# Kernel optimization log

Hardware: AMD Instinct MI355X
Metric: run time of the kernel (lower is better)

Reference implementation:

```python
import jax, jax.numpy as jnp
import numpy as np

B, T, E, H = 64, 577, 768, 64
GRID_H, GRID_W = 24, 24
NUM_PREFIX = 1
N = GRID_H * GRID_W  # 576 patches
EPS = 1e-5


def setup_inputs() -> dict:
    key = jax.random.key(0)
    ks = jax.random.split(key, 12)
    s = lambda k, shape, fan: jax.random.normal(k, shape, jnp.float32) / np.sqrt(fan)
    return {
        "x": jax.random.normal(ks[0], (B, T, E), jnp.float32),
        "w_q": s(ks[1], (E, H), E),
        "w_k": s(ks[2], (E, H), E),
        "w_v": s(ks[3], (E, H), E),
        "q_gamma": jnp.ones((H,), jnp.float32),
        "q_beta": jnp.zeros((H,), jnp.float32),
        "k_gamma": jnp.ones((H,), jnp.float32),
        "k_beta": jnp.zeros((H,), jnp.float32),
        "w_sigma": s(ks[4], (H, 2), H),
        "b_sigma": jnp.zeros((2,), jnp.float32),
        "w_alpha": s(ks[5], (H, 1), H),
        "b_alpha": jnp.zeros((1,), jnp.float32),
    }


def _layernorm(x, gamma, beta):
    mu = jnp.mean(x, axis=-1, keepdims=True)
    var = jnp.mean(jnp.square(x - mu), axis=-1, keepdims=True)
    return (x - mu) * jax.lax.rsqrt(var + EPS) * gamma + beta


def _grid_sq_dists():
    # coords[i] = (row, col) of patch i; squared coordinate differences [N, N]
    coords = jnp.stack(
        jnp.meshgrid(jnp.arange(GRID_H), jnp.arange(GRID_W), indexing="ij"), axis=-1
    ).reshape(N, 2).astype(jnp.float32)
    diff = coords[:, None, :] - coords[None, :, :]  # [N, N, 2]
    dy2 = jnp.square(diff[..., 0])  # row diff squared
    dx2 = jnp.square(diff[..., 1])  # col diff squared
    return dx2, dy2


def reference(x, w_q, w_k, w_v, q_gamma, q_beta, k_gamma, k_beta,
              w_sigma, b_sigma, w_alpha, b_alpha):
    q = _layernorm(x @ w_q, q_gamma, q_beta)  # [B, T, H]
    k = _layernorm(x @ w_k, k_gamma, k_beta)  # [B, T, H]
    v = x @ w_v                               # [B, T, H]

    sim = jnp.einsum("bqh,bkh->bqk", q, k)    # [B, T, T]

    q_nc = q[:, NUM_PREFIX:, :]               # [B, N, H]
    alpha = jax.nn.softplus(q_nc @ w_alpha + b_alpha)[..., 0]  # [B, N]
    sigma = jax.nn.sigmoid(q_nc @ w_sigma + b_sigma)           # [B, N, 2]
    sx = sigma[..., 0]  # [B, N]
    sy = sigma[..., 1]

    dx2, dy2 = _grid_sq_dists()  # [N, N] each
    # Gaussian decay bias: query-patch p controls sigma; [B, N, N]
    G = jnp.exp(
        -dx2[None] / (2.0 * jnp.square(sx)[:, :, None])
        - dy2[None] / (2.0 * jnp.square(sy)[:, :, None])
    )
    S = alpha[:, :, None] * G

    sim = sim.at[:, NUM_PREFIX:, NUM_PREFIX:].add(S)

    scale = jnp.sqrt(jnp.float32(H))
    attn = jax.nn.softmax(sim / scale, axis=-1)
    return attn @ v  # [B, T, H]
```

## Files before the change

kernel.cpp:

```cpp
#include <hip/hip_runtime.h>
#include <math.h>

#define B_ 64
#define T_ 577
#define E_ 768
#define H_ 64
#define N_ 576
#define GW_ 24

typedef float f32x4 __attribute__((ext_vector_type(4)));
typedef __bf16 bf16x8 __attribute__((ext_vector_type(8)));
typedef __bf16 bf16x4 __attribute__((ext_vector_type(4)));

__device__ inline void split_bf16(float f, __bf16& h, __bf16& l) {
  h = (__bf16)f;
  l = (__bf16)(f - (float)h);
}

__device__ inline float bperm_f(int byte_addr, float x) {
  return __int_as_float(__builtin_amdgcn_ds_bpermute(byte_addr, __float_as_int(x)));
}

#define GLOAD_LDS16(G, L)                                                     \
  __builtin_amdgcn_global_load_lds(                                           \
      (const __attribute__((address_space(1))) void*)(G),                     \
      (__attribute__((address_space(3))) void*)(L), 16, 0, 0)

__global__ __launch_bounds__(256) void prep_w_kernel(
    const float* __restrict__ wq, const float* __restrict__ wk, const float* __restrict__ wv,
    __bf16* __restrict__ wsw2)
{
  int t = blockIdx.x * 256 + threadIdx.x;
  if (t >= 24*192) return;
  int kc = t / 192, n = t - kc*192;
  const float* src = (n < 64) ? wq : ((n < 128) ? wk : wv);
  int nn = n & 63;
  int xb = (n & 3) ^ ((n >> 2) & 3);
  size_t cbase = (size_t)kc * 12288;
  #pragma unroll
  for (int g = 0; g < 4; ++g) {
    __bf16 hb[8], lb[8];
    #pragma unroll
    for (int j = 0; j < 8; ++j) {
      float f = src[(size_t)(kc*32 + g*8 + j)*64 + nn];
      split_bf16(f, hb[j], lb[j]);
    }
    int slot = n*4 + (g ^ xb);
    *(bf16x8*)(wsw2 + cbase + slot*8)        = *(bf16x8*)hb;
    *(bf16x8*)(wsw2 + cbase + 6144 + slot*8) = *(bf16x8*)lb;
  }
}

__global__ __launch_bounds__(256) void qkv_ln_kernel(
    const float* __restrict__ x, const __bf16* __restrict__ wsw2,
    const float* __restrict__ qg, const float* __restrict__ qb,
    const float* __restrict__ kg, const float* __restrict__ kb,
    const float* __restrict__ wsig, const float* __restrict__ bsig,
    const float* __restrict__ walp, const float* __restrict__ balp,
    float* __restrict__ qo, float* __restrict__ ko, float* __restrict__ vo,
    float* __restrict__ alo, float* __restrict__ sxo, float* __restrict__ syo)
{
  __shared__ __align__(16) float smem[64*193 + 256];
  __bf16* A_hi0 = (__bf16*)smem;
  __bf16* A_lo0 = A_hi0 + 2560;
  __bf16* A_hi1 = A_lo0 + 2560;
  __bf16* A_lo1 = A_hi1 + 2560;
  __bf16* B0    = A_lo1 + 2560;
  float (*Cs)[193] = (float (*)[193])smem;
  float* mu_q = smem + 64*193;
  float* rs_q = mu_q + 64;
  float* mu_k = rs_q + 64;
  float* rs_k = mu_k + 64;

  const int tid  = threadIdx.x;
  const int lane = tid & 63;
  const int w    = tid >> 6;
  const int quad = lane >> 4;
  const int m    = lane & 15;
  const int rowbase = blockIdx.x << 6;

  f32x4 acc[4][3];
  #pragma unroll
  for (int mt = 0; mt < 4; ++mt)
    #pragma unroll
    for (int nt = 0; nt < 3; ++nt)
      acc[mt][nt] = (f32x4){0.f, 0.f, 0.f, 0.f};

  const int kfrag = quad * 8;
  const int xl    = quad ^ (m & 3) ^ (m >> 2);

  float4 xr0, xr1;
  const int arow0 = tid >> 3,         ak0 = (tid & 7) * 4;
  const int arow1 = (tid + 256) >> 3, ak1 = (tid & 7) * 4;

  auto load_A = [&](int kc) {
    xr0 = *(const float4*)(x + (size_t)(rowbase + arow0)*E_ + kc*32 + ak0);
    xr1 = *(const float4*)(x + (size_t)(rowbase + arow1)*E_ + kc*32 + ak1);
  };
  auto store_A_to = [&](__bf16* AH, __bf16* AL) {
    __bf16 h0,l0,h1,l1,h2,l2,h3,l3;
    split_bf16(xr0.x,h0,l0); split_bf16(xr0.y,h1,l1);
    split_bf16(xr0.z,h2,l2); split_bf16(xr0.w,h3,l3);
    *(bf16x4*)&AH[arow0*40 + ak0] = (bf16x4){h0,h1,h2,h3};
    *(bf16x4*)&AL[arow0*40 + ak0] = (bf16x4){l0,l1,l2,l3};
    split_bf16(xr1.x,h0,l0); split_bf16(xr1.y,h1,l1);
    split_bf16(xr1.z,h2,l2); split_bf16(xr1.w,h3,l3);
    *(bf16x4*)&AH[arow1*40 + ak1] = (bf16x4){h0,h1,h2,h3};
    *(bf16x4*)&AL[arow1*40 + ak1] = (bf16x4){l0,l1,l2,l3};
  };
  auto issue_B = [&](int kc) {
    const size_t roff = (size_t)w * 1536;
    const __bf16* s_hi = wsw2 + (size_t)kc*12288 + roff + lane*8;
    const __bf16* s_lo = s_hi + 6144;
    __bf16* d_hi = B0 + roff;
    __bf16* d_lo = d_hi + 6144;
    #pragma unroll
    for (int j = 0; j < 3; ++j) {
      GLOAD_LDS16(s_hi + j*512, d_hi + j*512);
      GLOAD_LDS16(s_lo + j*512, d_lo + j*512);
    }
  };

  issue_B(0);
  load_A(0);
  store_A_to(A_hi0, A_lo0);
  load_A(1);
  __syncthreads();

  __bf16 *cA_hi = A_hi0, *cA_lo = A_lo0, *nA_hi = A_hi1, *nA_lo = A_lo1;

  #pragma unroll 1
  for (int kc = 0; kc < 24; ++kc) {
    bf16x8 bh[3], bl[3];
    #pragma unroll
    for (int nt = 0; nt < 3; ++nt) {
      int slotb = (w*48 + nt*16 + m)*4 + xl;
      bh[nt] = *(const bf16x8*)&B0[slotb*8];
      bl[nt] = *(const bf16x8*)&B0[6144 + slotb*8];
    }
    if (kc < 23) store_A_to(nA_hi, nA_lo);
    asm volatile("s_waitcnt lgkmcnt(0)" ::: "memory");
    __builtin_amdgcn_sched_barrier(0);
    if (kc < 23) issue_B(kc + 1);
    if (kc < 22) load_A(kc + 2);

    #pragma unroll
    for (int mt = 0; mt < 4; ++mt) {
      bf16x8 ah = *(const bf16x8*)&cA_hi[(mt*16 + m)*40 + kfrag];
      bf16x8 al = *(const bf16x8*)&cA_lo[(mt*16 + m)*40 + kfrag];
      #pragma unroll
      for (int nt = 0; nt < 3; ++nt) {
        acc[mt][nt] = __builtin_amdgcn_mfma_f32_16x16x32_bf16(ah, bh[nt], acc[mt][nt], 0, 0, 0);
        acc[mt][nt] = __builtin_amdgcn_mfma_f32_16x16x32_bf16(al, bh[nt], acc[mt][nt], 0, 0, 0);
        acc[mt][nt] = __builtin_amdgcn_mfma_f32_16x16x32_bf16(ah, bl[nt], acc[mt][nt], 0, 0, 0);
      }
    }
    __syncthreads();
    __bf16* t;
    t = cA_hi; cA_hi = nA_hi; nA_hi = t;
    t = cA_lo; cA_lo = nA_lo; nA_lo = t;
  }

  #pragma unroll
  for (int mt = 0; mt < 4; ++mt)
    #pragma unroll
    for (int nt = 0; nt < 3; ++nt) {
      int row = mt*16 + quad*4;
      int col = w*48 + nt*16 + m;
      Cs[row + 0][col] = acc[mt][nt].x;
      Cs[row + 1][col] = acc[mt][nt].y;
      Cs[row + 2][col] = acc[mt][nt].z;
      Cs[row + 3][col] = acc[mt][nt].w;
    }
  __syncthreads();

  if (tid < 64) {
    float s = 0.f;
    for (int h = 0; h < 64; ++h) s += Cs[tid][h];
    float mu = s * (1.f/64.f);
    float vs = 0.f;
    for (int h = 0; h < 64; ++h) { float d = Cs[tid][h] - mu; vs += d*d; }
    mu_q[tid] = mu;
    rs_q[tid] = rsqrtf(vs*(1.f/64.f) + 1e-5f);
  } else if (tid < 128) {
    int r = tid - 64;
    float s = 0.f;
    for (int h = 0; h < 64; ++h) s += Cs[r][64+h];
    float mu = s * (1.f/64.f);
    float vs = 0.f;
    for (int h = 0; h < 64; ++h) { float d = Cs[r][64+h] - mu; vs += d*d; }
    mu_k[r] = mu;
    rs_k[r] = rsqrtf(vs*(1.f/64.f) + 1e-5f);
  }
  __syncthreads();

  if (tid >= 192) {
    int r = tid - 192;
    int mrow = rowbase + r;
    int tindex = mrow % T_;
    if (tindex >= 1) {
      int bb = mrow / T_;
      int g = tindex - 1;
      float mu = mu_q[r], rs = rs_q[r];
      float za = 0.f, z0 = 0.f, z1 = 0.f;
      for (int h = 0; h < 64; ++h) {
        float qv = (Cs[r][h] - mu) * rs * qg[h] + qb[h];
        za += qv * walp[h];
        z0 += qv * wsig[2*h];
        z1 += qv * wsig[2*h+1];
      }
      za += balp[0]; z0 += bsig[0]; z1 += bsig[1];
      float al = fmaxf(za, 0.f) + log1pf(__expf(-fabsf(za)));
      float sx = 1.f/(1.f + __expf(-z0));
      float sy = 1.f/(1.f + __expf(-z1));
      alo[bb*N_ + g] = al;
      sxo[bb*N_ + g] = 0.5f/(sx*sx);
      syo[bb*N_ + g] = 0.5f/(sy*sy);
    }
  }
  for (int idx = tid; idx < 64*48; idx += 256) {
    int r = idx / 48, c4 = (idx - (idx/48)*48) * 4;
    size_t row = (size_t)rowbase + r;
    float4 val = make_float4(Cs[r][c4], Cs[r][c4+1], Cs[r][c4+2], Cs[r][c4+3]);
    if (c4 < 64) {
      float mu = mu_q[r], rs = rs_q[r];
      float4 o;
      o.x = (val.x - mu)*rs*qg[c4+0] + qb[c4+0];
      o.y = (val.y - mu)*rs*qg[c4+1] + qb[c4+1];
      o.z = (val.z - mu)*rs*qg[c4+2] + qb[c4+2];
      o.w = (val.w - mu)*rs*qg[c4+3] + qb[c4+3];
      *(float4*)(qo + row*64 + c4) = o;
    } else if (c4 < 128) {
      int h = c4 - 64;
      float mu = mu_k[r], rs = rs_k[r];
      float4 o;
      o.x = (val.x - mu)*rs*kg[h+0] + kb[h+0];
      o.y = (val.y - mu)*rs*kg[h+1] + kb[h+1];
      o.z = (val.z - mu)*rs*kg[h+2] + kb[h+2];
      o.w = (val.w - mu)*rs*kg[h+3] + kb[h+3];
      *(float4*)(ko + row*64 + h) = o;
    } else {
      *(float4*)(vo + row*64 + (c4-128)) = val;
    }
  }
}

__global__ __launch_bounds__(256, 4) void attn_kernel(
    const float* __restrict__ q, const float* __restrict__ k, const float* __restrict__ v,
    const float* __restrict__ ala, const float* __restrict__ sxa, const float* __restrict__ sya,
    float* __restrict__ out)
{
  __shared__ __align__(16) __bf16 sm[4*4608];
  __bf16* KH = sm;            __bf16* KL = sm + 4608;
  __bf16* VH = sm + 2*4608;   __bf16* VL = sm + 3*4608;

  const int tid  = threadIdx.x;
  const int lane = tid & 63;
  const int w    = tid >> 6;
  const int quad = lane >> 4;
  const int m    = lane & 15;

  const int f       = blockIdx.y * 10 + blockIdx.x;
  const int logical = (f & 7) * 80 + (f >> 3);
  const int b       = logical / 10;
  const int qt      = logical - b * 10;

  const float* qbase = q + (size_t)b * T_ * H_;
  const float* kbase = k + (size_t)b * T_ * H_;
  const float* vbase = v + (size_t)b * T_ * H_;

  const int  row    = qt*64 + w*16 + m;
  const int  rowc   = row < T_ ? row : T_ - 1;
  const bool qvalid = row < T_;
  const bool qhas   = (row >= 1) && qvalid;
  float al = 0.f, isx = 0.f, isy = 0.f, qr = 0.f, qc = 0.f;
  {
    int g = qhas ? row - 1 : 0;
    if (qhas) {
      al  = ala[b*N_ + g] * 0.125f;
      isx = sxa[b*N_ + g];
      isy = sya[b*N_ + g];
      int gr = g / GW_;
      qr = (float)gr;
      qc = (float)(g - gr*GW_);
    }
  }

  bf16x8 qh[2], ql[2];
  #pragma unroll
  for (int ks = 0; ks < 2; ++ks) {
    float4 f0 = *(const float4*)(qbase + (size_t)rowc*H_ + ks*32 + quad*8);
    float4 f1 = *(const float4*)(qbase + (size_t)rowc*H_ + ks*32 + quad*8 + 4);
    float fv[8] = {f0.x, f0.y, f0.z, f0.w, f1.x, f1.y, f1.z, f1.w};
    #pragma unroll
    for (int j = 0; j < 8; ++j) {
      float s = fv[j] * 0.125f;
      __bf16 h, l;
      split_bf16(s, h, l);
      qh[ks][j] = h;
      ql[ks][j] = l;
    }
  }

  float mo = -INFINITY, lsum = 0.f;
  f32x4 acc[4];
  #pragma unroll
  for (int nt = 0; nt < 4; ++nt) acc[nt] = (f32x4){0.f, 0.f, 0.f, 0.f};

  const int  addrA = ((2*(quad & 1))*16 + m) * 4;
  const int  addrB = addrA + 64;
  const bool hiNT  = quad >= 2;

  float4 kreg[4];
  float  vreg[16];
  const int d0 = tid & 15, k0 = (tid >> 4) * 4;

  auto load_kv = [&](int kt) {
    #pragma unroll
    for (int i = 0; i < 4; ++i) {
      int s = tid + 256*i;
      int key = s >> 4, c4 = (s & 15)*4;
      int kgl = kt*64 + key;
      int kcl = kgl < T_ ? kgl : T_ - 1;
      kreg[i] = *(const float4*)(kbase + (size_t)kcl*H_ + c4);
    }
    #pragma unroll
    for (int di = 0; di < 4; ++di)
      #pragma unroll
      for (int ki = 0; ki < 4; ++ki) {
        int kgl = kt*64 + k0 + ki;
        int kcl = kgl < T_ ? kgl : T_ - 1;
        vreg[di*4+ki] = vbase[(size_t)kcl*H_ + d0 + 16*di];
      }
  };
  auto store_kv = [&]() {
    #pragma unroll
    for (int i = 0; i < 4; ++i) {
      int s = tid + 256*i;
      int key = s >> 4, c4 = (s & 15)*4;
      __bf16 h0,l0,h1,l1,h2,l2,h3,l3;
      split_bf16(kreg[i].x,h0,l0); split_bf16(kreg[i].y,h1,l1);
      split_bf16(kreg[i].z,h2,l2); split_bf16(kreg[i].w,h3,l3);
      *(bf16x4*)&KH[key*72 + c4] = (bf16x4){h0,h1,h2,h3};
      *(bf16x4*)&KL[key*72 + c4] = (bf16x4){l0,l1,l2,l3};
    }
    #pragma unroll
    for (int di = 0; di < 4; ++di) {
      int dim = d0 + 16*di;
      __bf16 h0,l0,h1,l1,h2,l2,h3,l3;
      split_bf16(vreg[di*4+0],h0,l0); split_bf16(vreg[di*4+1],h1,l1);
      split_bf16(vreg[di*4+2],h2,l2); split_bf16(vreg[di*4+3],h3,l3);
      *(bf16x4*)&VH[dim*72 + k0] = (bf16x4){h0,h1,h2,h3};
      *(bf16x4*)&VL[dim*72 + k0] = (bf16x4){l0,l1,l2,l3};
    }
  };

  load_kv(0);
  #pragma unroll 1
  for (int kt = 0; kt < 10; ++kt) {
    __syncthreads();
    store_kv();
    __syncthreads();
    if (kt < 9) load_kv(kt + 1);

    float s_[4][4];
    #pragma unroll
    for (int nt = 0; nt < 4; ++nt) {
      f32x4 sac = (f32x4){0.f, 0.f, 0.f, 0.f};
      #pragma unroll
      for (int ks = 0; ks < 2; ++ks) {
        const int ko_ = ks*32 + quad*8;
        bf16x8 kh = *(const bf16x8*)&KH[(nt*16 + m)*72 + ko_];
        bf16x8 kl = *(const bf16x8*)&KL[(nt*16 + m)*72 + ko_];
        sac = __builtin_amdgcn_mfma_f32_16x16x32_bf16(kh, qh[ks], sac, 0, 0, 0);
        sac = __builtin_amdgcn_mfma_f32_16x16x32_bf16(kl, qh[ks], sac, 0, 0, 0);
        sac = __builtin_amdgcn_mfma_f32_16x16x32_bf16(kh, ql[ks], sac, 0, 0, 0);
      }
      s_[nt][0] = sac.x; s_[nt][1] = sac.y; s_[nt][2] = sac.z; s_[nt][3] = sac.w;
    }

    #pragma unroll
    for (int nt = 0; nt < 4; ++nt) {
      #pragma unroll
      for (int reg = 0; reg < 4; ++reg) {
        int key = kt*64 + nt*16 + quad*4 + reg;
        float sval = s_[nt][reg];
        float kgf = (float)(key - 1);
        float krf = floorf(kgf * (1.0f/24.0f));
        float kcf = kgf - 24.f*krf;
        float dx = qc - kcf, dy = qr - krf;
        float bias = al * __expf(-(dx*dx*isx + dy*dy*isy));
        bool khas = (key >= 1) && (key < T_);
        sval += (khas && qhas) ? bias : 0.f;
        s_[nt][reg] = (key < T_) ? sval : -1e30f;
      }
    }

    float mx = s_[0][0];
    #pragma unroll
    for (int nt = 0; nt < 4; ++nt)
      #pragma unroll
      for (int reg = 0; reg < 4; ++reg)
        mx = fmaxf(mx, s_[nt][reg]);
    mx = fmaxf(mx, __shfl_xor(mx, 16, 64));
    mx = fmaxf(mx, __shfl_xor(mx, 32, 64));
    float mn = fmaxf(mo, mx);
    float sc = __expf(mo - mn);
    float lt = 0.f;
    #pragma unroll
    for (int nt = 0; nt < 4; ++nt)
      #pragma unroll
      for (int reg = 0; reg < 4; ++reg) {
        float p = __expf(s_[nt][reg] - mn);
        s_[nt][reg] = p;
        lt += p;
      }
    lt += __shfl_xor(lt, 16, 64);
    lt += __shfl_xor(lt, 32, 64);
    lsum = lsum*sc + lt;
    mo = mn;
    #pragma unroll
    for (int nt = 0; nt < 4; ++nt) {
      acc[nt].x *= sc; acc[nt].y *= sc; acc[nt].z *= sc; acc[nt].w *= sc;
    }

    bf16x8 fh[2], fl[2];
    #pragma unroll
    for (int ks = 0; ks < 2; ++ks) {
      #pragma unroll
      for (int reg = 0; reg < 4; ++reg) {
        float xa0 = bperm_f(addrA, s_[2*ks+0][reg]);
        float xa1 = bperm_f(addrA, s_[2*ks+1][reg]);
        float xb0 = bperm_f(addrB, s_[2*ks+0][reg]);
        float xb1 = bperm_f(addrB, s_[2*ks+1][reg]);
        float va = hiNT ? xa1 : xa0;
        float vb = hiNT ? xb1 : xb0;
        __bf16 h, l;
        split_bf16(va, h, l); fh[ks][reg]   = h; fl[ks][reg]   = l;
        split_bf16(vb, h, l); fh[ks][4+reg] = h; fl[ks][4+reg] = l;
      }
    }

    #pragma unroll
    for (int nt = 0; nt < 4; ++nt) {
      f32x4 c = acc[nt];
      #pragma unroll
      for (int ks = 0; ks < 2; ++ks) {
        const int ko_ = ks*32 + quad*8;
        bf16x8 vh = *(const bf16x8*)&VH[(nt*16 + m)*72 + ko_];
        bf16x8 vl = *(const bf16x8*)&VL[(nt*16 + m)*72 + ko_];
        c = __builtin_amdgcn_mfma_f32_16x16x32_bf16(vh, fh[ks], c, 0, 0, 0);
        c = __builtin_amdgcn_mfma_f32_16x16x32_bf16(vl, fh[ks], c, 0, 0, 0);
        c = __builtin_amdgcn_mfma_f32_16x16x32_bf16(vh, fl[ks], c, 0, 0, 0);
      }
      acc[nt] = c;
    }
  }

  if (qvalid) {
    float inv = 1.f / lsum;
    #pragma unroll
    for (int nt = 0; nt < 4; ++nt) {
      float4 o;
      o.x = acc[nt].x * inv;
      o.y = acc[nt].y * inv;
      o.z = acc[nt].z * inv;
      o.w = acc[nt].w * inv;
      *(float4*)(out + ((size_t)b*T_ + row)*H_ + nt*16 + quad*4) = o;
    }
  }
}

extern "C" void kernel_launch(void* const* d_in, const int* in_sizes, int n_in,
                              void* d_out, int out_size, void* d_ws, size_t ws_size,
                              hipStream_t stream) {
  const float* x      = (const float*)d_in[0];
  const float* wq     = (const float*)d_in[1];
  const float* wk     = (const float*)d_in[2];
  const float* wv     = (const float*)d_in[3];
  const float* qg     = (const float*)d_in[4];
  const float* qb     = (const float*)d_in[5];
  const float* kg     = (const float*)d_in[6];
  const float* kb     = (const float*)d_in[7];
  const float* wsig   = (const float*)d_in[8];
  const float* bsig   = (const float*)d_in[9];
  const float* walp   = (const float*)d_in[10];
  const float* balp   = (const float*)d_in[11];
  float* out = (float*)d_out;

  float* ws  = (float*)d_ws;
  const size_t nrow = (size_t)B_ * T_;
  float* qo  = ws;
  float* ko  = qo + nrow*H_;
  float* vo  = ko + nrow*H_;
  float* alo = vo + nrow*H_;
  float* sxo = alo + (size_t)B_*N_;
  float* syo = sxo + (size_t)B_*N_;
  __bf16* wsw2 = (__bf16*)(syo + (size_t)B_*N_);

  hipLaunchKernelGGL(prep_w_kernel, dim3(18), dim3(256), 0, stream,
                     wq, wk, wv, wsw2);
  hipLaunchKernelGGL(qkv_ln_kernel, dim3(577), dim3(256), 0, stream,
                     x, wsw2, qg, qb, kg, kb, wsig, bsig, walp, balp,
                     qo, ko, vo, alo, sxo, syo);
  hipLaunchKernelGGL(attn_kernel, dim3(10, B_), dim3(256), 0, stream,
                     qo, ko, vo, alo, sxo, syo, out);
}
```

Measured before the change: 288.5 us.

## Load x fragments straight to registers and double-buffer weight tiles in LDS

The QKV projection no longer stages the x tile through LDS. Each lane loads its MFMA fragment of x directly from global memory into registers, one chunk ahead, and splits it into hi/lo bf16 in registers. The weight tiles are double-buffered in LDS, and since each wave reads only its own slice, the per-iteration block barrier is dropped. This removes LDS writes for A and the block syncs, but each of the four waves now reads the full x tile on its own with narrower strided accesses, which raises global/L2 traffic. The launch bounds now also request three blocks per CU.

```diff
diff --git a/kernel.cpp b/kernel.cpp
--- a/kernel.cpp
+++ b/kernel.cpp
@@ -51,7 +51,7 @@
   }
 }
 
-__global__ __launch_bounds__(256) void qkv_ln_kernel(
+__global__ __launch_bounds__(256, 3) void qkv_ln_kernel(
     const float* __restrict__ x, const __bf16* __restrict__ wsw2,
     const float* __restrict__ qg, const float* __restrict__ qb,
     const float* __restrict__ kg, const float* __restrict__ kb,
@@ -61,11 +61,8 @@
     float* __restrict__ alo, float* __restrict__ sxo, float* __restrict__ syo)
 {
   __shared__ __align__(16) float smem[64*193 + 256];
-  __bf16* A_hi0 = (__bf16*)smem;
-  __bf16* A_lo0 = A_hi0 + 2560;
-  __bf16* A_hi1 = A_lo0 + 2560;
-  __bf16* A_lo1 = A_hi1 + 2560;
-  __bf16* B0    = A_lo1 + 2560;
+  __bf16* Bb0 = (__bf16*)smem;
+  __bf16* Bb1 = Bb0 + 12288;
   float (*Cs)[193] = (float (*)[193])smem;
   float* mu_q = smem + 64*193;
   float* rs_q = mu_q + 64;
@@ -86,33 +83,24 @@
     for (int nt = 0; nt < 3; ++nt)
       acc[mt][nt] = (f32x4){0.f, 0.f, 0.f, 0.f};
 
-  const int kfrag = quad * 8;
-  const int xl    = quad ^ (m & 3) ^ (m >> 2);
-
-  float4 xr0, xr1;
-  const int arow0 = tid >> 3,         ak0 = (tid & 7) * 4;
-  const int arow1 = (tid + 256) >> 3, ak1 = (tid & 7) * 4;
-
-  auto load_A = [&](int kc) {
-    xr0 = *(const float4*)(x + (size_t)(rowbase + arow0)*E_ + kc*32 + ak0);
-    xr1 = *(const float4*)(x + (size_t)(rowbase + arow1)*E_ + kc*32 + ak1);
+  const int xl = quad ^ (m & 3) ^ (m >> 2);
+  const float* xbase = x + (size_t)(rowbase + m)*E_ + quad*8;
+
+  float4 aA[8], aB[8];
+
+  auto load_A = [&](int kc, float4 (&ar)[8]) {
+    #pragma unroll
+    for (int mt = 0; mt < 4; ++mt) {
+      const float* xp = xbase + (size_t)mt*16*E_ + kc*32;
+      ar[mt*2+0] = *(const float4*)xp;
+      ar[mt*2+1] = *(const float4*)(xp + 4);
+    }
   };
-  auto store_A_to = [&](__bf16* AH, __bf16* AL) {
-    __bf16 h0,l0,h1,l1,h2,l2,h3,l3;
-    split_bf16(xr0.x,h0,l0); split_bf16(xr0.y,h1,l1);
-    split_bf16(xr0.z,h2,l2); split_bf16(xr0.w,h3,l3);
-    *(bf16x4*)&AH[arow0*40 + ak0] = (bf16x4){h0,h1,h2,h3};
-    *(bf16x4*)&AL[arow0*40 + ak0] = (bf16x4){l0,l1,l2,l3};
-    split_bf16(xr1.x,h0,l0); split_bf16(xr1.y,h1,l1);
-    split_bf16(xr1.z,h2,l2); split_bf16(xr1.w,h3,l3);
-    *(bf16x4*)&AH[arow1*40 + ak1] = (bf16x4){h0,h1,h2,h3};
-    *(bf16x4*)&AL[arow1*40 + ak1] = (bf16x4){l0,l1,l2,l3};
-  };
-  auto issue_B = [&](int kc) {
+  auto issue_B = [&](int kc, __bf16* Bbuf) {
     const size_t roff = (size_t)w * 1536;
     const __bf16* s_hi = wsw2 + (size_t)kc*12288 + roff + lane*8;
     const __bf16* s_lo = s_hi + 6144;
-    __bf16* d_hi = B0 + roff;
+    __bf16* d_hi = Bbuf + roff;
     __bf16* d_lo = d_hi + 6144;
     #pragma unroll
     for (int j = 0; j < 3; ++j) {
@@ -121,33 +109,34 @@
     }
   };
 
-  issue_B(0);
-  load_A(0);
-  store_A_to(A_hi0, A_lo0);
-  load_A(1);
-  __syncthreads();
-
-  __bf16 *cA_hi = A_hi0, *cA_lo = A_lo0, *nA_hi = A_hi1, *nA_lo = A_lo1;
-
-  #pragma unroll 1
-  for (int kc = 0; kc < 24; ++kc) {
+  auto chunk_body = [&](int kc, __bf16* Bcur, __bf16* Bnxt,
+                        float4 (&acur)[8], float4 (&anxt)[8]) {
+    asm volatile("s_waitcnt vmcnt(0)" ::: "memory");
     bf16x8 bh[3], bl[3];
     #pragma unroll
     for (int nt = 0; nt < 3; ++nt) {
       int slotb = (w*48 + nt*16 + m)*4 + xl;
-      bh[nt] = *(const bf16x8*)&B0[slotb*8];
-      bl[nt] = *(const bf16x8*)&B0[6144 + slotb*8];
-    }
-    if (kc < 23) store_A_to(nA_hi, nA_lo);
+      bh[nt] = *(const bf16x8*)&Bcur[slotb*8];
+      bl[nt] = *(const bf16x8*)&Bcur[6144 + slotb*8];
+    }
     asm volatile("s_waitcnt lgkmcnt(0)" ::: "memory");
     __builtin_amdgcn_sched_barrier(0);
-    if (kc < 23) issue_B(kc + 1);
-    if (kc < 22) load_A(kc + 2);
-
+    if (kc < 23) {
+      issue_B(kc + 1, Bnxt);
+      load_A(kc + 1, anxt);
+    }
     #pragma unroll
     for (int mt = 0; mt < 4; ++mt) {
-      bf16x8 ah = *(const bf16x8*)&cA_hi[(mt*16 + m)*40 + kfrag];
-      bf16x8 al = *(const bf16x8*)&cA_lo[(mt*16 + m)*40 + kfrag];
+      float fv[8] = {acur[mt*2+0].x, acur[mt*2+0].y, acur[mt*2+0].z, acur[mt*2+0].w,
+                     acur[mt*2+1].x, acur[mt*2+1].y, acur[mt*2+1].z, acur[mt*2+1].w};
+      bf16x8 ah, al;
+      #pragma unroll
+      for (int j = 0; j < 8; ++j) {
+        __bf16 h, l;
+        split_bf16(fv[j], h, l);
+        ah[j] = h;
+        al[j] = l;
+      }
       #pragma unroll
       for (int nt = 0; nt < 3; ++nt) {
         acc[mt][nt] = __builtin_amdgcn_mfma_f32_16x16x32_bf16(ah, bh[nt], acc[mt][nt], 0, 0, 0);
@@ -155,11 +144,16 @@
         acc[mt][nt] = __builtin_amdgcn_mfma_f32_16x16x32_bf16(ah, bl[nt], acc[mt][nt], 0, 0, 0);
       }
     }
-    __syncthreads();
-    __bf16* t;
-    t = cA_hi; cA_hi = nA_hi; nA_hi = t;
-    t = cA_lo; cA_lo = nA_lo; nA_lo = t;
-  }
+  };
+
+  issue_B(0, Bb0);
+  load_A(0, aA);
+  #pragma unroll 1
+  for (int kc2 = 0; kc2 < 24; kc2 += 2) {
+    chunk_body(kc2,     Bb0, Bb1, aA, aB);
+    chunk_body(kc2 + 1, Bb1, Bb0, aB, aA);
+  }
+  __syncthreads();
 
   #pragma unroll
   for (int mt = 0; mt < 4; ++mt)
```

Result: slower. 325.7 us (+12.9%).
